# Performance work log

Hardware: AMD Instinct MI355X
Metric: run time of the kernel (lower is better)

The kernel has to match this reference:

```python
import jax, jax.numpy as jnp
import numpy as np

DIV_COEF = 1.0
EPS = 1e-8  # torch.cosine_similarity default eps


def setup_inputs() -> dict:
    key = jax.random.key(0)
    id_ = jax.random.normal(key, (8192, 512), dtype=jnp.float32)
    return {"id": id_}


def reference(id):
    # cosine similarity via norm + GEMM (math identical to broadcast form)
    norms = jnp.linalg.norm(id, axis=1)                      # [N]
    dots = id @ id.T                                          # [N, N]
    sim = dots / jnp.maximum(norms[:, None] * norms[None, :], EPS)
    n = id.shape[0]
    # zero diagonal, clamp negatives to zero, mean over full NxN
    off_diag = 1.0 - jnp.eye(n, dtype=sim.dtype)
    id_sim = off_diag * sim
    l_id_div = jnp.mean(jnp.where(id_sim < 0, 0.0, id_sim))
    total_loss = DIV_COEF * l_id_div
    return (total_loss, l_id_div)
```

## Files before the change

### kernel.cpp

```cpp
#include <hip/hip_runtime.h>
#include <stdint.h>

#define NROWS 8192
#define KDIM  512
#define BM    128
#define BK    128
#define NKI   (KDIM / BK)
#define NT    (NROWS / BM)
#define NBLK  (NT * (NT + 1) / 2)

typedef __attribute__((ext_vector_type(4))) float f32x4;
typedef long i64;

__device__ __forceinline__ void async_copy16(const unsigned char* g, unsigned char* l) {
  __builtin_amdgcn_global_load_lds(
      (const __attribute__((address_space(1))) unsigned int*)g,
      (__attribute__((address_space(3))) unsigned int*)l,
      16, 0, 0);
}

__global__ __launch_bounds__(256) void prep_kernel(
    const float* __restrict__ src, unsigned char* __restrict__ dst,
    float* __restrict__ acc) {
  const int row  = blockIdx.x * 4 + (threadIdx.x >> 6);
  const int lane = threadIdx.x & 63;
  const float4 v0 = ((const float4*)src)[row * 128 + lane * 2];
  const float4 v1 = ((const float4*)src)[row * 128 + lane * 2 + 1];
  float ss = v0.x * v0.x + v0.y * v0.y + v0.z * v0.z + v0.w * v0.w
           + v1.x * v1.x + v1.y * v1.y + v1.z * v1.z + v1.w * v1.w;
  #pragma unroll
  for (int off = 32; off > 0; off >>= 1) ss += __shfl_down(ss, off);
  const float rn = 1.0f / sqrtf(__shfl(ss, 0));
  if (row == 0 && lane == 0) *acc = 0.0f;
  int pk0 = __builtin_amdgcn_cvt_pk_fp8_f32(v0.x * rn, v0.y * rn, 0, false);
  pk0     = __builtin_amdgcn_cvt_pk_fp8_f32(v0.z * rn, v0.w * rn, pk0, true);
  int pk1 = __builtin_amdgcn_cvt_pk_fp8_f32(v1.x * rn, v1.y * rn, 0, false);
  pk1     = __builtin_amdgcn_cvt_pk_fp8_f32(v1.z * rn, v1.w * rn, pk1, true);
  const int cg  = lane >> 1;
  const int win = cg >> 3;
  const int p   = (cg & 7) ^ (row & 7);
  const int hf  = (lane & 1) ^ ((row >> 3) & 1);
  uint2 o; o.x = (unsigned int)pk0; o.y = (unsigned int)pk1;
  ((uint2*)dst)[row * 64 + win * 16 + p * 2 + hf] = o;
}

__device__ __forceinline__ int tri_base(int b) {
  return b * NT - (b * (b - 1)) / 2;
}

__global__ __launch_bounds__(256) void sim_reduce_kernel(
    const unsigned char* __restrict__ idn, float* __restrict__ acc) {
  const int idx = blockIdx.x;
  const float Af = 2.0f * NT + 1.0f;
  int bi = (int)((Af - sqrtf(Af * Af - 8.0f * (float)idx)) * 0.5f);
  while (bi > 0 && tri_base(bi) > idx) bi--;
  while (tri_base(bi + 1) <= idx) bi++;
  const int bj = bi + (idx - tri_base(bi));

  __shared__ __align__(16) unsigned char As[2][BM * BK];
  __shared__ __align__(16) unsigned char Bs[2][BM * BK];

  const int tid  = threadIdx.x;
  const int lane = tid & 63;
  const int w    = tid >> 6;
  const int wr   = (w >> 1) * 64;
  const int wc   = (w & 1) * 64;
  const int q    = lane >> 4;
  const int r16  = lane & 15;
  const int rx   = r16 & 7;
  const int hq   = ((q & 1) ^ ((r16 >> 3) & 1)) * 8;

  f32x4 acc_f[4][4];
  #pragma unroll
  for (int i = 0; i < 4; i++)
    #pragma unroll
    for (int j = 0; j < 4; j++)
      acc_f[i][j] = (f32x4){0.f, 0.f, 0.f, 0.f};

  const unsigned char* gA = idn + (size_t)(bi * BM + (tid >> 3)) * KDIM + (tid & 7) * 16;
  const unsigned char* gB = idn + (size_t)(bj * BM + (tid >> 3)) * KDIM + (tid & 7) * 16;
  const int ldso = tid * 16;

  #pragma unroll
  for (int i = 0; i < 4; i++) async_copy16(gA + (size_t)i * 16384, &As[0][ldso + i * 4096]);
  #pragma unroll
  for (int i = 0; i < 4; i++) async_copy16(gB + (size_t)i * 16384, &Bs[0][ldso + i * 4096]);

  #pragma unroll
  for (int t = 0; t < NKI; ++t) {
    const int cs = t & 1;
    if (t + 1 < NKI) {
      const int ns = cs ^ 1;
      const int ko = (t + 1) * BK;
      #pragma unroll
      for (int i = 0; i < 4; i++)
        async_copy16(gA + ko + (size_t)i * 16384, &As[ns][ldso + i * 4096]);
      #pragma unroll
      for (int i = 0; i < 4; i++)
        async_copy16(gB + ko + (size_t)i * 16384, &Bs[ns][ldso + i * 4096]);
      asm volatile("s_waitcnt vmcnt(8)" ::: "memory");
    } else {
      asm volatile("s_waitcnt vmcnt(0)" ::: "memory");
    }
    asm volatile("s_barrier" ::: "memory");

    #pragma unroll
    for (int s = 0; s < 4; s++) {
      const int pos = ((2 * s + (q >> 1)) ^ rx) * 16 + hq;
      i64 a[4], b[4];
      #pragma unroll
      for (int mi = 0; mi < 4; mi++) {
        a[mi] = *(const i64*)&As[cs][(wr + mi * 16 + r16) * BK + pos];
        b[mi] = *(const i64*)&Bs[cs][(wc + mi * 16 + r16) * BK + pos];
      }
      #pragma unroll
      for (int mi = 0; mi < 4; mi++)
        #pragma unroll
        for (int ni = 0; ni < 4; ni++)
          acc_f[mi][ni] = __builtin_amdgcn_mfma_f32_16x16x32_fp8_fp8(
              a[mi], b[ni], acc_f[mi][ni], 0, 0, 0);
    }

    asm volatile("s_barrier" ::: "memory");
  }

  float local = 0.f;
  const bool diag = (bi == bj);
  #pragma unroll
  for (int mi = 0; mi < 4; mi++)
    #pragma unroll
    for (int ni = 0; ni < 4; ni++)
      #pragma unroll
      for (int rr = 0; rr < 4; rr++) {
        const int ri = wr + mi * 16 + q * 4 + rr;
        const int ci = wc + ni * 16 + r16;
        float v = fmaxf(acc_f[mi][ni][rr], 0.f);
        if (diag && ri == ci) v = 0.f;
        local += v;
      }

  #pragma unroll
  for (int off = 32; off > 0; off >>= 1) local += __shfl_down(local, off);
  __syncthreads();
  float* red = (float*)As;
  if (lane == 0) red[w] = local;
  __syncthreads();
  if (tid == 0) {
    float s = red[0] + red[1] + red[2] + red[3];
    if (!diag) s *= 2.f;
    atomicAdd(acc, s);
  }
}

__global__ void finalize_kernel(const float* __restrict__ acc, float* __restrict__ out) {
  const float m = *acc * (1.0f / ((float)NROWS * (float)NROWS));
  out[0] = m;
  out[1] = m;
}

extern "C" void kernel_launch(void* const* d_in, const int* in_sizes, int n_in,
                              void* d_out, int out_size, void* d_ws, size_t ws_size,
                              hipStream_t stream) {
  const float* id = (const float*)d_in[0];
  float* out = (float*)d_out;
  unsigned char* idn = (unsigned char*)d_ws;
  float* acc = (float*)((char*)d_ws + (size_t)NROWS * KDIM);

  prep_kernel<<<NROWS / 4, 256, 0, stream>>>(id, idn, acc);
  sim_reduce_kernel<<<NBLK, 256, 0, stream>>>(idn, acc);
  finalize_kernel<<<1, 1, 0, stream>>>(acc, out);
}
```

Baseline: 98.13 us.

## Switch FP8 GEMM to MI355 scaled 32x32x64 MFMA with 128-bit LDS reads

Replaces the 16x16x32 FP8 MFMA tiling with the gfx950 scaled 32x32x64 f8f6f4 MFMA using unit scales. Each wave now computes 2x2 tiles of 32x32 with 16-wide accumulators and loads two 16-byte chunks per row instead of 8-byte pieces. The prep layout drops the half-swizzle to match the new wider reads. The aim is fewer MFMA issues and fewer, wider LDS loads per K step. The risk is LDS bank conflicts from the changed swizzle, plus the operand ordering having to match the instruction's lane layout.

New measurement: 98.75 us. No clear change (+0.6%).

```diff
diff --git a/kernel.cpp b/kernel.cpp
--- a/kernel.cpp
+++ b/kernel.cpp
@@ -9,8 +9,11 @@
 #define NT    (NROWS / BM)
 #define NBLK  (NT * (NT + 1) / 2)
 
-typedef __attribute__((ext_vector_type(4))) float f32x4;
-typedef long i64;
+typedef __attribute__((ext_vector_type(4)))  int   i32x4;
+typedef __attribute__((ext_vector_type(8)))  int   i32x8;
+typedef __attribute__((ext_vector_type(16))) float f32x16;
+
+#define SCALE1 0x7F7F7F7Fu
 
 __device__ __forceinline__ void async_copy16(const unsigned char* g, unsigned char* l) {
   __builtin_amdgcn_global_load_lds(
@@ -39,9 +42,8 @@
   const int cg  = lane >> 1;
   const int win = cg >> 3;
   const int p   = (cg & 7) ^ (row & 7);
-  const int hf  = (lane & 1) ^ ((row >> 3) & 1);
   uint2 o; o.x = (unsigned int)pk0; o.y = (unsigned int)pk1;
-  ((uint2*)dst)[row * 64 + win * 16 + p * 2 + hf] = o;
+  ((uint2*)dst)[row * 64 + win * 16 + p * 2 + (lane & 1)] = o;
 }
 
 __device__ __forceinline__ int tri_base(int b) {
@@ -65,17 +67,17 @@
   const int w    = tid >> 6;
   const int wr   = (w >> 1) * 64;
   const int wc   = (w & 1) * 64;
-  const int q    = lane >> 4;
-  const int r16  = lane & 15;
-  const int rx   = r16 & 7;
-  const int hq   = ((q & 1) ^ ((r16 >> 3) & 1)) * 8;
+  const int l31  = lane & 31;
+  const int kg   = lane >> 5;
+  const int key  = lane & 7;
 
-  f32x4 acc_f[4][4];
+  f32x16 acc_f[2][2];
   #pragma unroll
-  for (int i = 0; i < 4; i++)
+  for (int i = 0; i < 2; i++)
     #pragma unroll
-    for (int j = 0; j < 4; j++)
-      acc_f[i][j] = (f32x4){0.f, 0.f, 0.f, 0.f};
+    for (int j = 0; j < 2; j++)
+      #pragma unroll
+      for (int k = 0; k < 16; k++) acc_f[i][j][k] = 0.f;
 
   const unsigned char* gA = idn + (size_t)(bi * BM + (tid >> 3)) * KDIM + (tid & 7) * 16;
   const unsigned char* gB = idn + (size_t)(bj * BM + (tid >> 3)) * KDIM + (tid & 7) * 16;
@@ -105,20 +107,28 @@
     asm volatile("s_barrier" ::: "memory");
 
     #pragma unroll
-    for (int s = 0; s < 4; s++) {
-      const int pos = ((2 * s + (q >> 1)) ^ rx) * 16 + hq;
-      i64 a[4], b[4];
+    for (int s = 0; s < 2; s++) {
+      const int c0 = s * 4 + kg * 2;
+      const int pA0 = (c0 ^ key) * 16, pA1 = ((c0 + 1) ^ key) * 16;
+      i32x8 a[2], b[2];
       #pragma unroll
-      for (int mi = 0; mi < 4; mi++) {
-        a[mi] = *(const i64*)&As[cs][(wr + mi * 16 + r16) * BK + pos];
-        b[mi] = *(const i64*)&Bs[cs][(wc + mi * 16 + r16) * BK + pos];
+      for (int r = 0; r < 2; r++) {
+        const int rowA = (wr + r * 32 + l31) * BK;
+        const int rowB = (wc + r * 32 + l31) * BK;
+        i32x4 alo = *(const i32x4*)&As[cs][rowA + pA0];
+        i32x4 ahi = *(const i32x4*)&As[cs][rowA + pA1];
+        i32x4 blo = *(const i32x4*)&Bs[cs][rowB + pA0];
+        i32x4 bhi = *(const i32x4*)&Bs[cs][rowB + pA1];
+        a[r] = __builtin_shufflevector(alo, ahi, 0, 1, 2, 3, 4, 5, 6, 7);
+        b[r] = __builtin_shufflevector(blo, bhi, 0, 1, 2, 3, 4, 5, 6, 7);
       }
       #pragma unroll
-      for (int mi = 0; mi < 4; mi++)
+      for (int r = 0; r < 2; r++)
         #pragma unroll
-        for (int ni = 0; ni < 4; ni++)
-          acc_f[mi][ni] = __builtin_amdgcn_mfma_f32_16x16x32_fp8_fp8(
-              a[mi], b[ni], acc_f[mi][ni], 0, 0, 0);
+        for (int c = 0; c < 2; c++)
+          acc_f[r][c] = __builtin_amdgcn_mfma_scale_f32_32x32x64_f8f6f4(
+              a[r], b[c], acc_f[r][c], 0, 0,
+              0, SCALE1, 0, SCALE1);
     }
 
     asm volatile("s_barrier" ::: "memory");
@@ -127,14 +137,14 @@
   float local = 0.f;
   const bool diag = (bi == bj);
   #pragma unroll
-  for (int mi = 0; mi < 4; mi++)
+  for (int r = 0; r < 2; r++)
     #pragma unroll
-    for (int ni = 0; ni < 4; ni++)
+    for (int c = 0; c < 2; c++)
       #pragma unroll
-      for (int rr = 0; rr < 4; rr++) {
-        const int ri = wr + mi * 16 + q * 4 + rr;
-        const int ci = wc + ni * 16 + r16;
-        float v = fmaxf(acc_f[mi][ni][rr], 0.f);
+      for (int k = 0; k < 16; k++) {
+        const int ri = wr + r * 32 + (k & 3) + 8 * (k >> 2) + 4 * kg;
+        const int ci = wc + c * 32 + l31;
+        float v = fmaxf(acc_f[r][c][k], 0.f);
         if (diag && ri == ci) v = 0.f;
         local += v;
       }
```
